# Kernel optimization log

Measured on AMD Instinct MI355X. Metric: run time of the kernel, lower is better.

The kernel has to match this reference:

```python
import jax, jax.numpy as jnp
import numpy as np

RADIUS = 3
OX = 3
OI = 11
K_CLUST = 2
IMG = 30


def extract_patches(vol, radius):
    # vol: (N,N,N) -> (N,N,N,kd,kd,kd) windows from zero-padded volume
    p = jnp.pad(vol, radius)
    n = vol.shape[0]
    k = jnp.arange(2 * radius + 1)
    ii = jnp.arange(n)[:, None] + k[None, :]  # (N, kd)
    return p[ii[:, None, None, :, None, None],
             ii[None, :, None, None, :, None],
             ii[None, None, :, None, None, :]]


def setup_inputs() -> dict:
    key = jax.random.key(0)
    k1, k2 = jax.random.split(key)
    image = jax.random.normal(k1, (1, 1, IMG, IMG, IMG), dtype=jnp.float32)
    enc = jax.random.uniform(k2, (1, 2, IMG, IMG, IMG), dtype=jnp.float32)
    return {"image": image, "enc": enc}


def reference(image, enc):
    kd = 2 * RADIUS + 1
    img = jnp.mean(image, axis=1)[0]  # (30,30,30), batch_size=1

    # intensity affinity patches: exp(-(x_j - x_i)^2 / oi^2)
    P = extract_patches(img, RADIUS).reshape(-1, kd, kd, kd)  # (27000,7,7,7)
    center = P[:, RADIUS, RADIUS, RADIUS][:, None, None, None]
    Pg = jnp.exp(-(P - center) ** 2 / OI ** 2)

    # faithful to torch k_row construction: dw[i,j,l,m] = v[l]^2 + 2*v[m]^2
    # (independent of i,j); mask compares squared distance <= radius.
    v2 = ((jnp.arange(kd) - RADIUS) ** 2).astype(jnp.float32)
    dw2 = v2[:, None] + 2.0 * v2[None, :]  # (kd, kd) over (l, m)
    W2 = jnp.where(dw2 <= RADIUS, jnp.exp(-dw2 / OX ** 2), 0.0)
    # sum over the degenerate leading broadcast axis (i) -> factor kd,
    # broadcast over kd (b axis) to match weights[n, i, b, c, m] reduction.
    DWs = jnp.broadcast_to(kd * W2, (kd, kd, kd))  # (b, c, m)

    den_field = jnp.einsum('nbcm,bcm->n', Pg, DWs).reshape(img.shape)

    def assoc_ratio(e):
        S = extract_patches(e, RADIUS).reshape(-1, kd, kd, kd)
        nom_field = jnp.einsum('nbcm,nbcm,bcm->n', Pg, S, DWs).reshape(img.shape)
        return jnp.sum(e * nom_field) / jnp.sum(e * den_field)

    e0 = enc[0, 0]
    loss = jnp.mean(K_CLUST - (assoc_ratio(e0) + assoc_ratio(1.0 - e0)))
    return loss
```

## Files before the change

### kernel.cpp

```cpp
#include <hip/hip_runtime.h>

#define IMG 30
#define N3 (IMG * IMG * IMG)
#define THREADS 64
#define NBLK ((N3 + THREADS - 1) / THREADS)

__global__ __launch_bounds__(THREADS) void sncut_main(const float* __restrict__ img,
                                                      const float* __restrict__ e0,
                                                      double* __restrict__ partial) {
    const int n = blockIdx.x * blockDim.x + threadIdx.x;

    double a0 = 0.0, a1 = 0.0, b0 = 0.0, b1 = 0.0;

    if (n < N3) {
        const int z = n % IMG;
        const int y = (n / IMG) % IMG;
        const int x = n / (IMG * IMG);

        const float c = img[n];
        const float e = e0[n];
        const float inv_oi2 = 1.0f / 121.0f;

        const float w_e1 = 0.89483931681f;
        const float w_e2 = 0.80073740292f;
        const float w_e3 = 0.71653131057f;
        const float W[3][3] = {
            { w_e3, w_e1, w_e3 },
            { w_e2, 1.0f, w_e2 },
            { w_e3, w_e1, w_e3 },
        };

        float denIn = 0.0f;
        float nom0  = 0.0f;
        float wOOB  = 0.0f;

        #pragma unroll
        for (int db = -3; db <= 3; ++db) {
            const int nx = x + db;
            const bool xin = (unsigned)nx < (unsigned)IMG;
            #pragma unroll
            for (int dc = -1; dc <= 1; ++dc) {
                const int ny = y + dc;
                const bool yin = (unsigned)ny < (unsigned)IMG;
                #pragma unroll
                for (int dm = -1; dm <= 1; ++dm) {
                    const int nz = z + dm;
                    const bool zin = (unsigned)nz < (unsigned)IMG;
                    const float w = W[dc + 1][dm + 1];
                    if (xin && yin && zin) {
                        const int idx = (nx * IMG + ny) * IMG + nz;
                        const float p = img[idx];
                        const float d = p - c;
                        const float pg = expf(-d * d * inv_oi2);
                        const float wpg = w * pg;
                        denIn += wpg;
                        nom0  += wpg * e0[idx];
                    } else {
                        wOOB += w;
                    }
                }
            }
        }

        const float pgc  = expf(-c * c * inv_oi2);
        const float den  = denIn + wOOB * pgc;
        const float nom1 = denIn - nom0;

        a0 = (double)(e * nom0);
        a1 = (double)((1.0f - e) * nom1);
        b0 = (double)(e * den);
        b1 = (double)((1.0f - e) * den);
    }

    #pragma unroll
    for (int off = 32; off > 0; off >>= 1) {
        a0 += __shfl_down(a0, off, 64);
        a1 += __shfl_down(a1, off, 64);
        b0 += __shfl_down(b0, off, 64);
        b1 += __shfl_down(b1, off, 64);
    }
    if (threadIdx.x == 0) {
        partial[0 * NBLK + blockIdx.x] = a0;
        partial[1 * NBLK + blockIdx.x] = a1;
        partial[2 * NBLK + blockIdx.x] = b0;
        partial[3 * NBLK + blockIdx.x] = b1;
    }
}

__global__ __launch_bounds__(THREADS) void sncut_final(const double* __restrict__ partial,
                                                       float* __restrict__ out) {
    double a0 = 0.0, a1 = 0.0, b0 = 0.0, b1 = 0.0;
    for (int i = threadIdx.x; i < NBLK; i += THREADS) {
        a0 += partial[0 * NBLK + i];
        a1 += partial[1 * NBLK + i];
        b0 += partial[2 * NBLK + i];
        b1 += partial[3 * NBLK + i];
    }
    #pragma unroll
    for (int off = 32; off > 0; off >>= 1) {
        a0 += __shfl_down(a0, off, 64);
        a1 += __shfl_down(a1, off, 64);
        b0 += __shfl_down(b0, off, 64);
        b1 += __shfl_down(b1, off, 64);
    }
    if (threadIdx.x == 0) {
        out[0] = (float)(2.0 - a0 / b0 - a1 / b1);
    }
}

extern "C" void kernel_launch(void* const* d_in, const int* in_sizes, int n_in,
                              void* d_out, int out_size, void* d_ws, size_t ws_size,
                              hipStream_t stream) {
    const float* image = (const float*)d_in[0];
    const float* enc   = (const float*)d_in[1];
    float* out = (float*)d_out;
    double* partial = (double*)d_ws;

    sncut_main<<<NBLK, THREADS, 0, stream>>>(image, enc, partial);
    sncut_final<<<1, THREADS, 0, stream>>>(partial, out);
}
```

Measured before the change: 70.18 us.

## Fuse final reduction into main kernel via atomics and last-block finalize

Replaces the two-kernel reduction with a single kernel where each block atomically adds its partial sums to four global doubles, and the last block to increment a counter computes the final loss. A memset clears the accumulators before launch. This removes the second kernel launch, but adds a memset operation and contended double atomics from about 422 blocks. It also switches expf to the faster, less precise __expf intrinsic.

```diff
diff --git a/kernel.cpp b/kernel.cpp
--- a/kernel.cpp
+++ b/kernel.cpp
@@ -5,9 +5,11 @@
 #define THREADS 64
 #define NBLK ((N3 + THREADS - 1) / THREADS)
 
-__global__ __launch_bounds__(THREADS) void sncut_main(const float* __restrict__ img,
-                                                      const float* __restrict__ e0,
-                                                      double* __restrict__ partial) {
+__global__ __launch_bounds__(THREADS) void sncut_fused(const float* __restrict__ img,
+                                                       const float* __restrict__ e0,
+                                                       double* __restrict__ acc,
+                                                       unsigned* __restrict__ cnt,
+                                                       float* __restrict__ out) {
     const int n = blockIdx.x * blockDim.x + threadIdx.x;
 
     double a0 = 0.0, a1 = 0.0, b0 = 0.0, b1 = 0.0;
@@ -51,7 +53,7 @@
                         const int idx = (nx * IMG + ny) * IMG + nz;
                         const float p = img[idx];
                         const float d = p - c;
-                        const float pg = expf(-d * d * inv_oi2);
+                        const float pg = __expf(-d * d * inv_oi2);
                         const float wpg = w * pg;
                         denIn += wpg;
                         nom0  += wpg * e0[idx];
@@ -62,7 +64,7 @@
             }
         }
 
-        const float pgc  = expf(-c * c * inv_oi2);
+        const float pgc  = __expf(-c * c * inv_oi2);
         const float den  = denIn + wOOB * pgc;
         const float nom1 = denIn - nom0;
 
@@ -79,32 +81,21 @@
         b0 += __shfl_down(b0, off, 64);
         b1 += __shfl_down(b1, off, 64);
     }
+
     if (threadIdx.x == 0) {
-        partial[0 * NBLK + blockIdx.x] = a0;
-        partial[1 * NBLK + blockIdx.x] = a1;
-        partial[2 * NBLK + blockIdx.x] = b0;
-        partial[3 * NBLK + blockIdx.x] = b1;
-    }
-}
-
-__global__ __launch_bounds__(THREADS) void sncut_final(const double* __restrict__ partial,
-                                                       float* __restrict__ out) {
-    double a0 = 0.0, a1 = 0.0, b0 = 0.0, b1 = 0.0;
-    for (int i = threadIdx.x; i < NBLK; i += THREADS) {
-        a0 += partial[0 * NBLK + i];
-        a1 += partial[1 * NBLK + i];
-        b0 += partial[2 * NBLK + i];
-        b1 += partial[3 * NBLK + i];
-    }
-    #pragma unroll
-    for (int off = 32; off > 0; off >>= 1) {
-        a0 += __shfl_down(a0, off, 64);
-        a1 += __shfl_down(a1, off, 64);
-        b0 += __shfl_down(b0, off, 64);
-        b1 += __shfl_down(b1, off, 64);
-    }
-    if (threadIdx.x == 0) {
-        out[0] = (float)(2.0 - a0 / b0 - a1 / b1);
+        atomicAdd(&acc[0], a0);
+        atomicAdd(&acc[1], a1);
+        atomicAdd(&acc[2], b0);
+        atomicAdd(&acc[3], b1);
+        __threadfence();
+        const unsigned old = atomicAdd(cnt, 1u);
+        if (old == NBLK - 1) {
+            const double A0 = atomicAdd(&acc[0], 0.0);
+            const double A1 = atomicAdd(&acc[1], 0.0);
+            const double B0 = atomicAdd(&acc[2], 0.0);
+            const double B1 = atomicAdd(&acc[3], 0.0);
+            out[0] = (float)(2.0 - A0 / B0 - A1 / B1);
+        }
     }
 }
 
@@ -114,8 +105,10 @@
     const float* image = (const float*)d_in[0];
     const float* enc   = (const float*)d_in[1];
     float* out = (float*)d_out;
-    double* partial = (double*)d_ws;
+    double* acc = (double*)d_ws;
+    unsigned* cnt = (unsigned*)((char*)d_ws + 32);
 
-    sncut_main<<<NBLK, THREADS, 0, stream>>>(image, enc, partial);
-    sncut_final<<<1, THREADS, 0, stream>>>(partial, out);
+    hipMemsetAsync(d_ws, 0, 64, stream);
+
+    sncut_fused<<<NBLK, THREADS, 0, stream>>>(image, enc, acc, cnt, out);
 }
```

Result: slower. 88.66 us (+26.3%).
